# Performance work log

Hardware: AMD Instinct MI355X
Metric: run time of the kernel (lower is better)

The kernel has to match this reference:

```python
import jax, jax.numpy as jnp
import numpy as np

# ---- module constants (from init_kwargs) ----
EMBED_DIM = 384
NUM_HYPEREDGES = 128
TOPK = 64
SPATIAL_SHAPE = (16, 32, 32)  # D, H, W -> N = 16384
SPACING = (2.0, 1.0, 1.0)
SPATIAL_WEIGHT = 0.1
B, N, C = 4, 16 * 32 * 32, EMBED_DIM


def _l2norm(x, axis=-1, eps=1e-12):
    n = jnp.linalg.norm(x, axis=axis, keepdims=True)
    return x / jnp.maximum(n, eps)


def _get_3d_coords():
    D, H, W = SPATIAL_SHAPE
    z = jnp.arange(D, dtype=jnp.float32) * SPACING[0]
    y = jnp.arange(H, dtype=jnp.float32) * SPACING[1]
    x = jnp.arange(W, dtype=jnp.float32) * SPACING[2]
    zz, yy, xx = jnp.meshgrid(z, y, x, indexing='ij')
    return jnp.stack([zz, yy, xx], axis=-1).reshape(-1, 3)  # (N, 3)


def setup_inputs() -> dict:
    key = jax.random.key(0)
    k1, k2 = jax.random.split(key)
    node_features = jax.random.normal(k1, (B, N, C), dtype=jnp.float32)
    class_token = jax.random.normal(k2, (1, 1, C), dtype=jnp.float32)
    temperature = jnp.ones((1,), dtype=jnp.float32) * 0.07
    return {"node_features": node_features, "class_token": class_token, "temperature": temperature}


def reference(node_features, class_token, temperature):
    Ne = NUM_HYPEREDGES
    w = SPATIAL_WEIGHT
    temp = temperature[0]

    nodes_n = _l2norm(node_features)                      # (B, N, C)

    # Step 1: center sampling by semantic similarity to class token
    ct_n = _l2norm(jnp.broadcast_to(class_token, (B, 1, C)))
    scores = jnp.einsum('boc,bnc->bn', ct_n, nodes_n) / temp  # (B, N)
    _, center_idx = jax.lax.top_k(scores, Ne)             # (B, Ne)

    # Gather centers and compute cosine sim of every center vs all nodes
    centers = jnp.take_along_axis(node_features, center_idx[:, :, None], axis=1)  # (B, Ne, C)
    centers_n = _l2norm(centers)
    sem_sim = jnp.einsum('bec,bnc->ben', centers_n, nodes_n) / temp  # (B, Ne, N)

    # Spatial bias (normalized distance from each center voxel)
    coords = _get_3d_coords()                             # (N, 3)
    center_coords = coords[center_idx]                    # (B, Ne, 3)
    diff = coords[None, None, :, :] - center_coords[:, :, None, :]  # (B, Ne, N, 3)
    dist = jnp.linalg.norm(diff, axis=-1)                 # (B, Ne, N)
    dist = dist / (jnp.max(dist, axis=-1, keepdims=True) + 1e-8)
    combined = (1.0 - w) * sem_sim + w * (1.0 - dist)     # (B, Ne, N)

    # Per-hyperedge top-K neighbors -> incidence matrix H (B, N, Ne)
    _, nbr_idx = jax.lax.top_k(combined, TOPK)            # (B, Ne, K)
    b_ix = jnp.arange(B)[:, None, None]
    e_ix = jnp.arange(Ne)[None, :, None]
    Hmat = jnp.zeros((B, N, Ne), dtype=node_features.dtype)
    Hmat = Hmat.at[b_ix, nbr_idx, e_ix].set(1.0)
    return Hmat
```

## Files before the change

### kernel.cpp

```cpp
#include <hip/hip_runtime.h>
#include <math.h>

#define BB 4
#define NN 16384
#define CC 384
#define NE 128
#define KK 64
#define CAP 1024

typedef unsigned short ushort_t;
typedef __attribute__((ext_vector_type(8))) short bf16x8;
typedef __attribute__((ext_vector_type(4))) float f32x4;
#define MFMA(a, b, c) __builtin_amdgcn_mfma_f32_16x16x32_bf16(a, b, c, 0, 0, 0)

__device__ inline unsigned fkey(float f) {
    unsigned b = __float_as_uint(f);
    return (b & 0x80000000u) ? ~b : (b | 0x80000000u);
}
__device__ inline ushort_t bf16rne(float f) {
    unsigned u = __float_as_uint(f);
    unsigned r = u + 0x7FFFu + ((u >> 16) & 1u);
    return (ushort_t)(r >> 16);
}
__device__ inline float bf16tof(ushort_t h) {
    return __uint_as_float(((unsigned)h) << 16);
}
__device__ inline void cvt2(float fa, float fb, unsigned& hp, unsigned& lp) {
    unsigned ua = __float_as_uint(fa), ub = __float_as_uint(fb);
    unsigned ra = ua + 0x8000u, rb = ub + 0x8000u;
    hp = (ra >> 16) | (rb & 0xFFFF0000u);
    float ha = __uint_as_float(ra & 0xFFFF0000u);
    float hb = __uint_as_float(rb & 0xFFFF0000u);
    float la = fa - ha, lb = fb - hb;
    unsigned lra = __float_as_uint(la) + 0x8000u;
    unsigned lrb = __float_as_uint(lb) + 0x8000u;
    lp = (lra >> 16) | (lrb & 0xFFFF0000u);
}

__device__ inline void load_lds16(const ushort_t* g, ushort_t* l) {
    __builtin_amdgcn_global_load_lds(
        (const __attribute__((address_space(1))) unsigned int*)(const void*)g,
        (__attribute__((address_space(3))) unsigned int*)(void*)l, 16, 0, 0);
}

__device__ inline void bin_select4k(const unsigned* hist, int t, int* wsum,
                                    int* sh_bin, int* sh_r, int r) {
    int base = t * 4;
    int c0 = hist[base], c1 = hist[base + 1], c2 = hist[base + 2], c3 = hist[base + 3];
    int csum = c0 + c1 + c2 + c3;
    int lane = t & 63, wid = t >> 6;
    int x = csum;
#pragma unroll
    for (int off = 1; off < 64; off <<= 1) {
        int v = __shfl_down(x, off, 64);
        if (lane + off < 64) x += v;
    }
    if (lane == 0) wsum[wid] = x;
    __syncthreads();
    int after = 0;
    for (int w2 = wid + 1; w2 < 16; ++w2) after += wsum[w2];
    int S = x - csum + after;
    if (S < r && S + c3 >= r) { *sh_bin = base + 3; *sh_r = r - S; }
    S += c3;
    if (S < r && S + c2 >= r) { *sh_bin = base + 2; *sh_r = r - S; }
    S += c2;
    if (S < r && S + c1 >= r) { *sh_bin = base + 1; *sh_r = r - S; }
    S += c1;
    if (S < r && S + c0 >= r) { *sh_bin = base + 0; *sh_r = r - S; }
    __syncthreads();
}

__global__ __launch_bounds__(256) void k_scores(const float* __restrict__ nf,
                                                const float* __restrict__ ct,
                                                unsigned* __restrict__ keys,
                                                float* __restrict__ invn) {
    int wave = threadIdx.x >> 6;
    int lane = threadIdx.x & 63;
    float4 ta = ((const float4*)ct)[lane];
    float2 tc = ((const float2*)(ct + 256))[lane];
    for (int rg = blockIdx.x; rg < BB * NN / 4; rg += gridDim.x) {
        int row = rg * 4 + wave;
        const float* x = nf + (size_t)row * CC;
        float4 a  = ((const float4*)x)[lane];
        float2 c2 = ((const float2*)(x + 256))[lane];
        float ss = a.x*a.x + a.y*a.y + a.z*a.z + a.w*a.w + c2.x*c2.x + c2.y*c2.y;
        float dt = ta.x*a.x + ta.y*a.y + ta.z*a.z + ta.w*a.w + tc.x*c2.x + tc.y*c2.y;
#pragma unroll
        for (int off = 32; off; off >>= 1) {
            ss += __shfl_xor(ss, off, 64);
            dt += __shfl_xor(dt, off, 64);
        }
        if (lane == 0) {
            float inv = 1.0f / fmaxf(sqrtf(ss), 1e-12f);
            invn[row] = inv;
            keys[row] = fkey(dt * inv);
        }
    }
}

__global__ __launch_bounds__(1024) void k_top128(const unsigned* __restrict__ keys,
                                                 const float* __restrict__ nf,
                                                 const float* __restrict__ invn,
                                                 float* __restrict__ meta,
                                                 ushort_t* __restrict__ Ahi,
                                                 ushort_t* __restrict__ Alo) {
    __shared__ unsigned hist[4096];
    __shared__ int wsum[16];
    __shared__ int sh_bin, sh_r;
    __shared__ unsigned cu[NE];
    __shared__ int cil[NE];
    __shared__ unsigned eqk[CAP];
    __shared__ int eqi[CAP];
    __shared__ int cnt_gt, cnt_eq;
    __shared__ int ocid[NE];
    int b = blockIdx.x;
    int t = threadIdx.x;
    const uint4* rowv = (const uint4*)(keys + b * NN);
    if (t == 0) { cnt_gt = 0; cnt_eq = 0; }
    ((uint4*)hist)[t] = make_uint4(0, 0, 0, 0);
    __syncthreads();
    uint4 u0 = rowv[t], u1 = rowv[t + 1024], u2 = rowv[t + 2048], u3 = rowv[t + 3072];
    atomicAdd(&hist[u0.x >> 20], 1u); atomicAdd(&hist[u0.y >> 20], 1u);
    atomicAdd(&hist[u0.z >> 20], 1u); atomicAdd(&hist[u0.w >> 20], 1u);
    atomicAdd(&hist[u1.x >> 20], 1u); atomicAdd(&hist[u1.y >> 20], 1u);
    atomicAdd(&hist[u1.z >> 20], 1u); atomicAdd(&hist[u1.w >> 20], 1u);
    atomicAdd(&hist[u2.x >> 20], 1u); atomicAdd(&hist[u2.y >> 20], 1u);
    atomicAdd(&hist[u2.z >> 20], 1u); atomicAdd(&hist[u2.w >> 20], 1u);
    atomicAdd(&hist[u3.x >> 20], 1u); atomicAdd(&hist[u3.y >> 20], 1u);
    atomicAdd(&hist[u3.z >> 20], 1u); atomicAdd(&hist[u3.w >> 20], 1u);
    __syncthreads();
    bin_select4k(hist, t, wsum, &sh_bin, &sh_r, NE);
    unsigned bin = (unsigned)sh_bin;
    int r = sh_r;
#define EMIT128(uu, nn) { unsigned tb = (uu) >> 20; \
    if (tb > bin) { int p = atomicAdd(&cnt_gt, 1); cu[p] = (uu); cil[p] = (nn); } \
    else if (tb == bin) { int p = atomicAdd(&cnt_eq, 1); if (p < CAP) { eqk[p] = (uu); eqi[p] = (nn); } } }
    EMIT128(u0.x, 4*t+0); EMIT128(u0.y, 4*t+1); EMIT128(u0.z, 4*t+2); EMIT128(u0.w, 4*t+3);
    EMIT128(u1.x, 4096+4*t+0); EMIT128(u1.y, 4096+4*t+1); EMIT128(u1.z, 4096+4*t+2); EMIT128(u1.w, 4096+4*t+3);
    EMIT128(u2.x, 8192+4*t+0); EMIT128(u2.y, 8192+4*t+1); EMIT128(u2.z, 8192+4*t+2); EMIT128(u2.w, 8192+4*t+3);
    EMIT128(u3.x, 12288+4*t+0); EMIT128(u3.y, 12288+4*t+1); EMIT128(u3.z, 12288+4*t+2); EMIT128(u3.w, 12288+4*t+3);
#undef EMIT128
    __syncthreads();
    int ne = cnt_eq < CAP ? cnt_eq : CAP;
    for (int i = t; i < ne; i += 1024) {
        unsigned ki = eqk[i]; int ii = eqi[i], rk = 0;
        for (int j = 0; j < ne; ++j) {
            unsigned kj = eqk[j];
            rk += (kj > ki) || (kj == ki && eqi[j] < ii);
        }
        if (rk < r) { cu[cnt_gt + rk] = ki; cil[cnt_gt + rk] = ii; }
    }
    __syncthreads();
    if (t < NE) {
        unsigned mu = cu[t]; int mi = cil[t], rk = 0;
#pragma unroll 4
        for (int j = 0; j < NE; ++j) {
            unsigned ou = cu[j]; int oi = cil[j];
            rk += (ou > mu) || (ou == mu && oi < mi);
        }
        ocid[rk] = mi;
    }
    __syncthreads();
    if (t < NE) {
        int ci = ocid[t];
        float zc = (float)(ci >> 10) * 2.0f;
        float yc = (float)((ci >> 5) & 31);
        float xc = (float)(ci & 31);
        float mz = fmaxf(zc * zc, (30.f - zc) * (30.f - zc));
        float my = fmaxf(yc * yc, (31.f - yc) * (31.f - yc));
        float mx = fmaxf(xc * xc, (31.f - xc) * (31.f - xc));
        float md = sqrtf(mz + my + mx);
        int be = b * NE + t;
        meta[be * 4 + 0] = zc;
        meta[be * 4 + 1] = yc;
        meta[be * 4 + 2] = xc;
        meta[be * 4 + 3] = 1.0f / (md + 1e-8f);
    }
    {
        int wid2 = t >> 6, lane2 = t & 63;
        ushort_t* dh = Ahi + (size_t)b * NE * CC;
        ushort_t* dl = Alo + (size_t)b * NE * CC;
        for (int e = wid2; e < NE; e += 16) {
            int ci = ocid[e];
            float inv = invn[b * NN + ci];
            const float* src = nf + ((size_t)b * NN + ci) * CC;
            float4 a  = ((const float4*)src)[lane2];
            float2 cv = ((const float2*)(src + 256))[lane2];
            a.x *= inv; a.y *= inv; a.z *= inv; a.w *= inv;
            cv.x *= inv; cv.y *= inv;
            ushort4 h4; ushort2 h2;
            h4.x = bf16rne(a.x); h4.y = bf16rne(a.y); h4.z = bf16rne(a.z); h4.w = bf16rne(a.w);
            h2.x = bf16rne(cv.x); h2.y = bf16rne(cv.y);
            ushort4 l4; ushort2 l2;
            l4.x = bf16rne(a.x - bf16tof(h4.x)); l4.y = bf16rne(a.y - bf16tof(h4.y));
            l4.z = bf16rne(a.z - bf16tof(h4.z)); l4.w = bf16rne(a.w - bf16tof(h4.w));
            l2.x = bf16rne(cv.x - bf16tof(h2.x)); l2.y = bf16rne(cv.y - bf16tof(h2.y));
            int off4 = ((lane2 >> 1) * NE + e) * 8 + 4 * (lane2 & 1);
            int off2 = ((32 + (lane2 >> 2)) * NE + e) * 8 + 2 * (lane2 & 3);
            *(ushort4*)(dh + off4) = h4;
            *(ushort2*)(dh + off2) = h2;
            *(ushort4*)(dl + off4) = l4;
            *(ushort2*)(dl + off2) = l2;
        }
    }
}

__global__ __launch_bounds__(256, 2) void k_gemm(const float* __restrict__ nf,
                                                 const ushort_t* __restrict__ Ahi,
                                                 const ushort_t* __restrict__ Alo,
                                                 const float* __restrict__ invn,
                                                 const float* __restrict__ meta,
                                                 const float* __restrict__ temp,
                                                 unsigned* __restrict__ outk) {
    __shared__ ushort_t Ah[2][4096], Al[2][4096];
    __shared__ ushort_t Bh[2][4160], Bl[2][4160];
    __shared__ float ms[NE * 4];
    __shared__ float invs_s[128];
    int b  = blockIdx.y;
    int n0 = blockIdx.x * 128;
    int t  = threadIdx.x;
    int w = t >> 6, lane = t & 63, quad = lane >> 4, mrow = lane & 15;
    int wr = w >> 1, wc = w & 1;
    for (int i = t; i < NE * 4; i += 256) ms[i] = meta[b * NE * 4 + i];
    if (t < 128) invs_s[t] = invn[b * NN + n0 + t];
    f32x4 acc[4][4];
#pragma unroll
    for (int i = 0; i < 4; ++i)
#pragma unroll
        for (int j = 0; j < 4; ++j) acc[i][j] = (f32x4)0.f;
    const ushort_t* Abh = Ahi + (size_t)b * NE * CC;
    const ushort_t* Abl = Alo + (size_t)b * NE * CC;
    const ushort_t* ah0 = Abh + w * 1024 + lane * 8;
    const ushort_t* ah1 = ah0 + 512;
    const ushort_t* al0 = Abl + w * 1024 + lane * 8;
    const ushort_t* al1 = al0 + 512;
    int bn = t >> 2, bk8 = t & 3;
    int sb0 = bk8 * 130 + bn, sb1 = sb0 + 64;
    const float* bs0 = nf + ((size_t)b * NN + n0 + bn) * CC + bk8 * 8;
    const float* bs1 = bs0 + (size_t)64 * CC;
    float4 s0a, s0b, s0c, s0d;
    float4 s1a, s1b, s1c, s1d;
    load_lds16(ah0, &Ah[0][w * 1024]);
    load_lds16(ah1, &Ah[0][w * 1024 + 512]);
    load_lds16(al0, &Al[0][w * 1024]);
    load_lds16(al1, &Al[0][w * 1024 + 512]);
    __builtin_amdgcn_sched_barrier(0);
    s0a = ((const float4*)bs0)[0]; s0b = ((const float4*)bs0)[1];
    s0c = ((const float4*)bs1)[0]; s0d = ((const float4*)bs1)[1];
    s1a = ((const float4*)(bs0 + 32))[0]; s1b = ((const float4*)(bs0 + 32))[1];
    s1c = ((const float4*)(bs1 + 32))[0]; s1d = ((const float4*)(bs1 + 32))[1];
    {
        uint4 ph, pl;
        cvt2(s0a.x, s0a.y, ph.x, pl.x); cvt2(s0a.z, s0a.w, ph.y, pl.y);
        cvt2(s0b.x, s0b.y, ph.z, pl.z); cvt2(s0b.z, s0b.w, ph.w, pl.w);
        *(uint4*)&Bh[0][sb0 * 8] = ph; *(uint4*)&Bl[0][sb0 * 8] = pl;
        cvt2(s0c.x, s0c.y, ph.x, pl.x); cvt2(s0c.z, s0c.w, ph.y, pl.y);
        cvt2(s0d.x, s0d.y, ph.z, pl.z); cvt2(s0d.z, s0d.w, ph.w, pl.w);
        *(uint4*)&Bh[0][sb1 * 8] = ph; *(uint4*)&Bl[0][sb1 * 8] = pl;
    }
    s0a = ((const float4*)(bs0 + 64))[0]; s0b = ((const float4*)(bs0 + 64))[1];
    s0c = ((const float4*)(bs1 + 64))[0]; s0d = ((const float4*)(bs1 + 64))[1];
    asm volatile("s_waitcnt vmcnt(8) lgkmcnt(0)" ::: "memory");
    __builtin_amdgcn_s_barrier();
    __builtin_amdgcn_sched_barrier(0);

#define GSTEP(KS, CUR, NXT, SA, SB, SC, SD)                                     \
    {                                                                           \
        if ((KS) < 11) {                                                        \
            const int kt = ((KS) + 1) * 32;                                     \
            load_lds16(ah0 + kt * 128, &Ah[NXT][w * 1024]);                     \
            load_lds16(ah1 + kt * 128, &Ah[NXT][w * 1024 + 512]);               \
            load_lds16(al0 + kt * 128, &Al[NXT][w * 1024]);                     \
            load_lds16(al1 + kt * 128, &Al[NXT][w * 1024 + 512]);               \
            __builtin_amdgcn_sched_barrier(0);                                  \
            uint4 ph, pl;                                                       \
            cvt2(SA.x, SA.y, ph.x, pl.x); cvt2(SA.z, SA.w, ph.y, pl.y);         \
            cvt2(SB.x, SB.y, ph.z, pl.z); cvt2(SB.z, SB.w, ph.w, pl.w);         \
            *(uint4*)&Bh[NXT][sb0 * 8] = ph; *(uint4*)&Bl[NXT][sb0 * 8] = pl;   \
            cvt2(SC.x, SC.y, ph.x, pl.x); cvt2(SC.z, SC.w, ph.y, pl.y);         \
            cvt2(SD.x, SD.y, ph.z, pl.z); cvt2(SD.z, SD.w, ph.w, pl.w);         \
            *(uint4*)&Bh[NXT][sb1 * 8] = ph; *(uint4*)&Bl[NXT][sb1 * 8] = pl;   \
            const int kt3 = ((KS) + 3 <= 11 ? (KS) + 3 : 11) * 32;              \
            SA = ((const float4*)(bs0 + kt3))[0];                               \
            SB = ((const float4*)(bs0 + kt3))[1];                               \
            SC = ((const float4*)(bs1 + kt3))[0];                               \
            SD = ((const float4*)(bs1 + kt3))[1];                               \
        }                                                                       \
        bf16x8 afh[4], afl[4], bfh[4], bfl[4];                                  \
        _Pragma("unroll") for (int i = 0; i < 4; ++i) {                         \
            int m = wr * 64 + i * 16 + mrow;                                    \
            afh[i] = *(const bf16x8*)&Ah[CUR][(quad * 128 + m) * 8];            \
            afl[i] = *(const bf16x8*)&Al[CUR][(quad * 128 + m) * 8];            \
        }                                                                       \
        _Pragma("unroll") for (int j = 0; j < 4; ++j) {                         \
            int n = wc * 64 + j * 16 + mrow;                                    \
            bfh[j] = *(const bf16x8*)&Bh[CUR][(quad * 130 + n) * 8];            \
            bfl[j] = *(const bf16x8*)&Bl[CUR][(quad * 130 + n) * 8];            \
        }                                                                       \
        __builtin_amdgcn_s_setprio(1);                                          \
        _Pragma("unroll") for (int i = 0; i < 4; ++i)                           \
        _Pragma("unroll") for (int j = 0; j < 4; ++j) {                         \
            acc[i][j] = MFMA(afh[i], bfh[j], acc[i][j]);                        \
            acc[i][j] = MFMA(afh[i], bfl[j], acc[i][j]);                        \
            acc[i][j] = MFMA(afl[i], bfh[j], acc[i][j]);                        \
        }                                                                       \
        __builtin_amdgcn_s_setprio(0);                                          \
        if ((KS) < 11) {                                                        \
            asm volatile("s_waitcnt vmcnt(8) lgkmcnt(0)" ::: "memory");         \
            __builtin_amdgcn_s_barrier();                                       \
            __builtin_amdgcn_sched_barrier(0);                                  \
        }                                                                       \
    }

    GSTEP(0, 0, 1, s1a, s1b, s1c, s1d)
    GSTEP(1, 1, 0, s0a, s0b, s0c, s0d)
    GSTEP(2, 0, 1, s1a, s1b, s1c, s1d)
    GSTEP(3, 1, 0, s0a, s0b, s0c, s0d)
    GSTEP(4, 0, 1, s1a, s1b, s1c, s1d)
    GSTEP(5, 1, 0, s0a, s0b, s0c, s0d)
    GSTEP(6, 0, 1, s1a, s1b, s1c, s1d)
    GSTEP(7, 1, 0, s0a, s0b, s0c, s0d)
    GSTEP(8, 0, 1, s1a, s1b, s1c, s1d)
    GSTEP(9, 1, 0, s0a, s0b, s0c, s0d)
    GSTEP(10, 0, 1, s1a, s1b, s1c, s1d)
    GSTEP(11, 1, 0, s0a, s0b, s0c, s0d)
#undef GSTEP

    float scale = 0.9f / temp[0];
#pragma unroll
    for (int j = 0; j < 4; ++j) {
        int nloc = wc * 64 + j * 16 + mrow;
        int n = n0 + nloc;
        float invnn = invs_s[nloc];
        float zf = (float)(n >> 10) * 2.0f;
        float yf = (float)((n >> 5) & 31);
        float xf = (float)(n & 31);
#pragma unroll
        for (int i = 0; i < 4; ++i) {
#pragma unroll
            for (int r = 0; r < 4; ++r) {
                int el = wr * 64 + i * 16 + quad * 4 + r;
                float zc = ms[el * 4 + 0], yc = ms[el * 4 + 1], xc = ms[el * 4 + 2], ivd = ms[el * 4 + 3];
                float dz = zf - zc, dy = yf - yc, dx = xf - xc;
                float dist = sqrtf(dz * dz + dy * dy + dx * dx);
                float v = scale * invnn * acc[i][j][r] + 0.1f * (1.0f - dist * ivd);
                outk[((size_t)(b * NE + el)) * NN + n] = fkey(v);
            }
        }
    }
}

__global__ __launch_bounds__(1024) void k_top64(const unsigned* __restrict__ comb,
                                                unsigned* __restrict__ bmg) {
    __shared__ unsigned hist[4096];
    __shared__ unsigned bm[512];
    __shared__ int wsum[16];
    __shared__ int sh_bin, sh_r;
    __shared__ unsigned eqk[CAP];
    __shared__ int eqi[CAP];
    __shared__ int cnt_eq;
    int be = blockIdx.x;
    int t  = threadIdx.x;
    const uint4* rowv = (const uint4*)(comb + (size_t)be * NN);
    if (t == 0) cnt_eq = 0;
    ((uint4*)hist)[t] = make_uint4(0, 0, 0, 0);
    if (t < 128) ((uint4*)bm)[t] = make_uint4(0, 0, 0, 0);
    __syncthreads();
    uint4 u0 = rowv[t], u1 = rowv[t + 1024], u2 = rowv[t + 2048], u3 = rowv[t + 3072];
    atomicAdd(&hist[u0.x >> 20], 1u); atomicAdd(&hist[u0.y >> 20], 1u);
    atomicAdd(&hist[u0.z >> 20], 1u); atomicAdd(&hist[u0.w >> 20], 1u);
    atomicAdd(&hist[u1.x >> 20], 1u); atomicAdd(&hist[u1.y >> 20], 1u);
    atomicAdd(&hist[u1.z >> 20], 1u); atomicAdd(&hist[u1.w >> 20], 1u);
    atomicAdd(&hist[u2.x >> 20], 1u); atomicAdd(&hist[u2.y >> 20], 1u);
    atomicAdd(&hist[u2.z >> 20], 1u); atomicAdd(&hist[u2.w >> 20], 1u);
    atomicAdd(&hist[u3.x >> 20], 1u); atomicAdd(&hist[u3.y >> 20], 1u);
    atomicAdd(&hist[u3.z >> 20], 1u); atomicAdd(&hist[u3.w >> 20], 1u);
    __syncthreads();
    bin_select4k(hist, t, wsum, &sh_bin, &sh_r, KK);
    unsigned bin = (unsigned)sh_bin;
    int r = sh_r;
#define EMIT64(uu, nn) { unsigned tb = (uu) >> 20; \
    if (tb > bin) { atomicOr(&bm[(nn) >> 5], 1u << ((nn) & 31)); } \
    else if (tb == bin) { int p = atomicAdd(&cnt_eq, 1); if (p < CAP) { eqk[p] = (uu); eqi[p] = (nn); } } }
    EMIT64(u0.x, 4*t+0); EMIT64(u0.y, 4*t+1); EMIT64(u0.z, 4*t+2); EMIT64(u0.w, 4*t+3);
    EMIT64(u1.x, 4096+4*t+0); EMIT64(u1.y, 4096+4*t+1); EMIT64(u1.z, 4096+4*t+2); EMIT64(u1.w, 4096+4*t+3);
    EMIT64(u2.x, 8192+4*t+0); EMIT64(u2.y, 8192+4*t+1); EMIT64(u2.z, 8192+4*t+2); EMIT64(u2.w, 8192+4*t+3);
    EMIT64(u3.x, 12288+4*t+0); EMIT64(u3.y, 12288+4*t+1); EMIT64(u3.z, 12288+4*t+2); EMIT64(u3.w, 12288+4*t+3);
#undef EMIT64
    __syncthreads();
    int ne = cnt_eq < CAP ? cnt_eq : CAP;
    for (int i = t; i < ne; i += 1024) {
        unsigned ki = eqk[i]; int ii = eqi[i], rk = 0;
        for (int j = 0; j < ne; ++j) {
            unsigned kj = eqk[j];
            rk += (kj > ki) || (kj == ki && eqi[j] < ii);
        }
        if (rk < r) atomicOr(&bm[ii >> 5], 1u << (ii & 31));
    }
    __syncthreads();
    if (t < 128) ((uint4*)(bmg + (size_t)be * 512))[t] = ((uint4*)bm)[t];
}

__global__ __launch_bounds__(256) void k_expand(const unsigned* __restrict__ bmg,
                                                float* __restrict__ H) {
    __shared__ unsigned wl[256];
    int b  = blockIdx.y;
    int n0 = blockIdx.x * 64;
    int t  = threadIdx.x;
    int w0 = n0 >> 5;
    wl[t] = bmg[((size_t)b * NE + (t >> 1)) * 512 + w0 + (t & 1)];
    __syncthreads();
    float4* dst = (float4*)(H + ((size_t)b * NN + n0) * NE);
#pragma unroll
    for (int i = 0; i < 8; ++i) {
        int flat = t + 256 * i;
        int nl = flat >> 5, f4 = flat & 31;
        int wsel = nl >> 5, bit = nl & 31;
        int e = f4 * 4;
        float4 v;
        v.x = (float)((wl[(e + 0) * 2 + wsel] >> bit) & 1u);
        v.y = (float)((wl[(e + 1) * 2 + wsel] >> bit) & 1u);
        v.z = (float)((wl[(e + 2) * 2 + wsel] >> bit) & 1u);
        v.w = (float)((wl[(e + 3) * 2 + wsel] >> bit) & 1u);
        dst[flat] = v;
    }
}

extern "C" void kernel_launch(void* const* d_in, const int* in_sizes, int n_in,
                              void* d_out, int out_size, void* d_ws, size_t ws_size,
                              hipStream_t stream) {
    const float* nf   = (const float*)d_in[0];
    const float* ct   = (const float*)d_in[1];
    const float* temp = (const float*)d_in[2];
    float* out = (float*)d_out;

    unsigned* keys = (unsigned*)d_ws;
    float* invn    = (float*)(keys + BB * NN);
    float* meta    = invn + BB * NN;
    ushort_t* Ahi  = (ushort_t*)(meta + BB * NE * 4);
    ushort_t* Alo  = Ahi + (size_t)BB * NE * CC;
    unsigned* bmg  = (unsigned*)(Alo + (size_t)BB * NE * CC);

    k_scores <<<2048, 256, 0, stream>>>(nf, ct, keys, invn);
    k_top128 <<<BB, 1024, 0, stream>>>(keys, nf, invn, meta, Ahi, Alo);
    k_gemm   <<<dim3(NN / 128, BB), 256, 0, stream>>>(nf, Ahi, Alo, invn, meta, temp, (unsigned*)out);
    k_top64  <<<BB * NE, 1024, 0, stream>>>((const unsigned*)out, bmg);
    k_expand <<<dim3(NN / 64, BB), 256, 0, stream>>>(bmg, out);
}
```

Baseline: 245.3 us.

## Pre-split node features into bf16 hi/lo tiles in k_scores, stream into GEMM via LDS loads

k_scores, which already reads every node row, now also splits each fp32 feature into bf16 hi/lo parts and writes them to workspace in the exact tiled layout the GEMM consumes. k_gemm then loads both A and B operands with direct global-to-LDS loads and no longer does in-loop conversion or register staging. The aim is to take conversion ALU work and scattered fp32 loads off the GEMM's critical path. The cost is extra global writes of the hi/lo copies (same byte count as the fp32 input), which k_gemm reads back. The wait now drains all outstanding loads (vmcnt(0)) at each step.

Result: slower. 309.6 us (+26.2%).

```diff
diff --git a/kernel.cpp b/kernel.cpp
--- a/kernel.cpp
+++ b/kernel.cpp
@@ -73,11 +73,15 @@
 __global__ __launch_bounds__(256) void k_scores(const float* __restrict__ nf,
                                                 const float* __restrict__ ct,
                                                 unsigned* __restrict__ keys,
-                                                float* __restrict__ invn) {
+                                                float* __restrict__ invn,
+                                                ushort_t* __restrict__ Bhi,
+                                                ushort_t* __restrict__ Blo) {
     int wave = threadIdx.x >> 6;
     int lane = threadIdx.x & 63;
     float4 ta = ((const float4*)ct)[lane];
     float2 tc = ((const float2*)(ct + 256))[lane];
+    int off4 = ((lane >> 1) * 128) * 8 + 4 * (lane & 1);
+    int off2 = ((32 + (lane >> 2)) * 128) * 8 + 2 * (lane & 3);
     for (int rg = blockIdx.x; rg < BB * NN / 4; rg += gridDim.x) {
         int row = rg * 4 + wave;
         const float* x = nf + (size_t)row * CC;
@@ -95,6 +99,18 @@
             invn[row] = inv;
             keys[row] = fkey(dt * inv);
         }
+        uint2 h4, l4; unsigned h2, l2;
+        cvt2(a.x, a.y, h4.x, l4.x);
+        cvt2(a.z, a.w, h4.y, l4.y);
+        cvt2(c2.x, c2.y, h2, l2);
+        int bq = row >> 14;
+        int n  = row & (NN - 1);
+        int nt = n >> 7, nl = n & 127;
+        size_t tb = ((size_t)(bq * 128 + nt)) * 49152;
+        *(uint2*)(Bhi + tb + off4 + nl * 8) = h4;
+        *(uint2*)(Blo + tb + off4 + nl * 8) = l4;
+        *(unsigned*)(Bhi + tb + off2 + nl * 8) = h2;
+        *(unsigned*)(Blo + tb + off2 + nl * 8) = l2;
     }
 }
 
@@ -205,19 +221,21 @@
     }
 }
 
-__global__ __launch_bounds__(256, 2) void k_gemm(const float* __restrict__ nf,
-                                                 const ushort_t* __restrict__ Ahi,
+__global__ __launch_bounds__(256, 2) void k_gemm(const ushort_t* __restrict__ Ahi,
                                                  const ushort_t* __restrict__ Alo,
+                                                 const ushort_t* __restrict__ Bhi,
+                                                 const ushort_t* __restrict__ Blo,
                                                  const float* __restrict__ invn,
                                                  const float* __restrict__ meta,
                                                  const float* __restrict__ temp,
                                                  unsigned* __restrict__ outk) {
     __shared__ ushort_t Ah[2][4096], Al[2][4096];
-    __shared__ ushort_t Bh[2][4160], Bl[2][4160];
+    __shared__ ushort_t Bh[2][4096], Bl[2][4096];
     __shared__ float ms[NE * 4];
     __shared__ float invs_s[128];
     int b  = blockIdx.y;
-    int n0 = blockIdx.x * 128;
+    int bx = blockIdx.x;
+    int n0 = bx * 128;
     int t  = threadIdx.x;
     int w = t >> 6, lane = t & 63, quad = lane >> 4, mrow = lane & 15;
     int wr = w >> 1, wc = w & 1;
@@ -228,104 +246,67 @@
     for (int i = 0; i < 4; ++i)
 #pragma unroll
         for (int j = 0; j < 4; ++j) acc[i][j] = (f32x4)0.f;
-    const ushort_t* Abh = Ahi + (size_t)b * NE * CC;
-    const ushort_t* Abl = Alo + (size_t)b * NE * CC;
-    const ushort_t* ah0 = Abh + w * 1024 + lane * 8;
-    const ushort_t* ah1 = ah0 + 512;
-    const ushort_t* al0 = Abl + w * 1024 + lane * 8;
-    const ushort_t* al1 = al0 + 512;
-    int bn = t >> 2, bk8 = t & 3;
-    int sb0 = bk8 * 130 + bn, sb1 = sb0 + 64;
-    const float* bs0 = nf + ((size_t)b * NN + n0 + bn) * CC + bk8 * 8;
-    const float* bs1 = bs0 + (size_t)64 * CC;
-    float4 s0a, s0b, s0c, s0d;
-    float4 s1a, s1b, s1c, s1d;
-    load_lds16(ah0, &Ah[0][w * 1024]);
-    load_lds16(ah1, &Ah[0][w * 1024 + 512]);
-    load_lds16(al0, &Al[0][w * 1024]);
-    load_lds16(al1, &Al[0][w * 1024 + 512]);
-    __builtin_amdgcn_sched_barrier(0);
-    s0a = ((const float4*)bs0)[0]; s0b = ((const float4*)bs0)[1];
-    s0c = ((const float4*)bs1)[0]; s0d = ((const float4*)bs1)[1];
-    s1a = ((const float4*)(bs0 + 32))[0]; s1b = ((const float4*)(bs0 + 32))[1];
-    s1c = ((const float4*)(bs1 + 32))[0]; s1d = ((const float4*)(bs1 + 32))[1];
-    {
-        uint4 ph, pl;
-        cvt2(s0a.x, s0a.y, ph.x, pl.x); cvt2(s0a.z, s0a.w, ph.y, pl.y);
-        cvt2(s0b.x, s0b.y, ph.z, pl.z); cvt2(s0b.z, s0b.w, ph.w, pl.w);
-        *(uint4*)&Bh[0][sb0 * 8] = ph; *(uint4*)&Bl[0][sb0 * 8] = pl;
-        cvt2(s0c.x, s0c.y, ph.x, pl.x); cvt2(s0c.z, s0c.w, ph.y, pl.y);
-        cvt2(s0d.x, s0d.y, ph.z, pl.z); cvt2(s0d.z, s0d.w, ph.w, pl.w);
-        *(uint4*)&Bh[0][sb1 * 8] = ph; *(uint4*)&Bl[0][sb1 * 8] = pl;
-    }
-    s0a = ((const float4*)(bs0 + 64))[0]; s0b = ((const float4*)(bs0 + 64))[1];
-    s0c = ((const float4*)(bs1 + 64))[0]; s0d = ((const float4*)(bs1 + 64))[1];
-    asm volatile("s_waitcnt vmcnt(8) lgkmcnt(0)" ::: "memory");
+    const ushort_t* Asrh = Ahi + (size_t)b * NE * CC + w * 1024 + lane * 8;
+    const ushort_t* Asrl = Alo + (size_t)b * NE * CC + w * 1024 + lane * 8;
+    const ushort_t* Bsrh = Bhi + ((size_t)(b * 128 + bx)) * 49152 + w * 1024 + lane * 8;
+    const ushort_t* Bsrl = Blo + ((size_t)(b * 128 + bx)) * 49152 + w * 1024 + lane * 8;
+    int ld0 = w * 1024, ld1 = w * 1024 + 512;
+    load_lds16(Asrh,       &Ah[0][ld0]);
+    load_lds16(Asrh + 512, &Ah[0][ld1]);
+    load_lds16(Asrl,       &Al[0][ld0]);
+    load_lds16(Asrl + 512, &Al[0][ld1]);
+    load_lds16(Bsrh,       &Bh[0][ld0]);
+    load_lds16(Bsrh + 512, &Bh[0][ld1]);
+    load_lds16(Bsrl,       &Bl[0][ld0]);
+    load_lds16(Bsrl + 512, &Bl[0][ld1]);
+    asm volatile("s_waitcnt vmcnt(0)" ::: "memory");
     __builtin_amdgcn_s_barrier();
     __builtin_amdgcn_sched_barrier(0);
-
-#define GSTEP(KS, CUR, NXT, SA, SB, SC, SD)                                     \
-    {                                                                           \
-        if ((KS) < 11) {                                                        \
-            const int kt = ((KS) + 1) * 32;                                     \
-            load_lds16(ah0 + kt * 128, &Ah[NXT][w * 1024]);                     \
-            load_lds16(ah1 + kt * 128, &Ah[NXT][w * 1024 + 512]);               \
-            load_lds16(al0 + kt * 128, &Al[NXT][w * 1024]);                     \
-            load_lds16(al1 + kt * 128, &Al[NXT][w * 1024 + 512]);               \
-            __builtin_amdgcn_sched_barrier(0);                                  \
-            uint4 ph, pl;                                                       \
-            cvt2(SA.x, SA.y, ph.x, pl.x); cvt2(SA.z, SA.w, ph.y, pl.y);         \
-            cvt2(SB.x, SB.y, ph.z, pl.z); cvt2(SB.z, SB.w, ph.w, pl.w);         \
-            *(uint4*)&Bh[NXT][sb0 * 8] = ph; *(uint4*)&Bl[NXT][sb0 * 8] = pl;   \
-            cvt2(SC.x, SC.y, ph.x, pl.x); cvt2(SC.z, SC.w, ph.y, pl.y);         \
-            cvt2(SD.x, SD.y, ph.z, pl.z); cvt2(SD.z, SD.w, ph.w, pl.w);         \
-            *(uint4*)&Bh[NXT][sb1 * 8] = ph; *(uint4*)&Bl[NXT][sb1 * 8] = pl;   \
-            const int kt3 = ((KS) + 3 <= 11 ? (KS) + 3 : 11) * 32;              \
-            SA = ((const float4*)(bs0 + kt3))[0];                               \
-            SB = ((const float4*)(bs0 + kt3))[1];                               \
-            SC = ((const float4*)(bs1 + kt3))[0];                               \
-            SD = ((const float4*)(bs1 + kt3))[1];                               \
-        }                                                                       \
-        bf16x8 afh[4], afl[4], bfh[4], bfl[4];                                  \
-        _Pragma("unroll") for (int i = 0; i < 4; ++i) {                         \
-            int m = wr * 64 + i * 16 + mrow;                                    \
-            afh[i] = *(const bf16x8*)&Ah[CUR][(quad * 128 + m) * 8];            \
-            afl[i] = *(const bf16x8*)&Al[CUR][(quad * 128 + m) * 8];            \
-        }                                                                       \
-        _Pragma("unroll") for (int j = 0; j < 4; ++j) {                         \
-            int n = wc * 64 + j * 16 + mrow;                                    \
-            bfh[j] = *(const bf16x8*)&Bh[CUR][(quad * 130 + n) * 8];            \
-            bfl[j] = *(const bf16x8*)&Bl[CUR][(quad * 130 + n) * 8];            \
-        }                                                                       \
-        __builtin_amdgcn_s_setprio(1);                                          \
-        _Pragma("unroll") for (int i = 0; i < 4; ++i)                           \
-        _Pragma("unroll") for (int j = 0; j < 4; ++j) {                         \
-            acc[i][j] = MFMA(afh[i], bfh[j], acc[i][j]);                        \
-            acc[i][j] = MFMA(afh[i], bfl[j], acc[i][j]);                        \
-            acc[i][j] = MFMA(afl[i], bfh[j], acc[i][j]);                        \
-        }                                                                       \
-        __builtin_amdgcn_s_setprio(0);                                          \
-        if ((KS) < 11) {                                                        \
-            asm volatile("s_waitcnt vmcnt(8) lgkmcnt(0)" ::: "memory");         \
-            __builtin_amdgcn_s_barrier();                                       \
-            __builtin_amdgcn_sched_barrier(0);                                  \
-        }                                                                       \
-    }
-
-    GSTEP(0, 0, 1, s1a, s1b, s1c, s1d)
-    GSTEP(1, 1, 0, s0a, s0b, s0c, s0d)
-    GSTEP(2, 0, 1, s1a, s1b, s1c, s1d)
-    GSTEP(3, 1, 0, s0a, s0b, s0c, s0d)
-    GSTEP(4, 0, 1, s1a, s1b, s1c, s1d)
-    GSTEP(5, 1, 0, s0a, s0b, s0c, s0d)
-    GSTEP(6, 0, 1, s1a, s1b, s1c, s1d)
-    GSTEP(7, 1, 0, s0a, s0b, s0c, s0d)
-    GSTEP(8, 0, 1, s1a, s1b, s1c, s1d)
-    GSTEP(9, 1, 0, s0a, s0b, s0c, s0d)
-    GSTEP(10, 0, 1, s1a, s1b, s1c, s1d)
-    GSTEP(11, 1, 0, s0a, s0b, s0c, s0d)
-#undef GSTEP
-
+    int cur = 0;
+    for (int ks = 0; ks < 12; ++ks) {
+        int nxt = cur ^ 1;
+        if (ks < 11) {
+            int so = (ks + 1) * 4096;
+            load_lds16(Asrh + so,       &Ah[nxt][ld0]);
+            load_lds16(Asrh + so + 512, &Ah[nxt][ld1]);
+            load_lds16(Asrl + so,       &Al[nxt][ld0]);
+            load_lds16(Asrl + so + 512, &Al[nxt][ld1]);
+            load_lds16(Bsrh + so,       &Bh[nxt][ld0]);
+            load_lds16(Bsrh + so + 512, &Bh[nxt][ld1]);
+            load_lds16(Bsrl + so,       &Bl[nxt][ld0]);
+            load_lds16(Bsrl + so + 512, &Bl[nxt][ld1]);
+            __builtin_amdgcn_sched_barrier(0);
+        }
+        bf16x8 afh[4], afl[4], bfh[4], bfl[4];
+#pragma unroll
+        for (int i = 0; i < 4; ++i) {
+            int m = wr * 64 + i * 16 + mrow;
+            afh[i] = *(const bf16x8*)&Ah[cur][(quad * 128 + m) * 8];
+            afl[i] = *(const bf16x8*)&Al[cur][(quad * 128 + m) * 8];
+        }
+#pragma unroll
+        for (int j = 0; j < 4; ++j) {
+            int n = wc * 64 + j * 16 + mrow;
+            bfh[j] = *(const bf16x8*)&Bh[cur][(quad * 128 + n) * 8];
+            bfl[j] = *(const bf16x8*)&Bl[cur][(quad * 128 + n) * 8];
+        }
+        __builtin_amdgcn_s_setprio(1);
+#pragma unroll
+        for (int i = 0; i < 4; ++i)
+#pragma unroll
+            for (int j = 0; j < 4; ++j) {
+                acc[i][j] = MFMA(afh[i], bfh[j], acc[i][j]);
+                acc[i][j] = MFMA(afh[i], bfl[j], acc[i][j]);
+                acc[i][j] = MFMA(afl[i], bfh[j], acc[i][j]);
+            }
+        __builtin_amdgcn_s_setprio(0);
+        if (ks < 11) {
+            asm volatile("s_waitcnt vmcnt(0) lgkmcnt(0)" ::: "memory");
+            __builtin_amdgcn_s_barrier();
+            __builtin_amdgcn_sched_barrier(0);
+        }
+        cur = nxt;
+    }
     float scale = 0.9f / temp[0];
 #pragma unroll
     for (int j = 0; j < 4; ++j) {
@@ -440,10 +421,12 @@
     ushort_t* Ahi  = (ushort_t*)(meta + BB * NE * 4);
     ushort_t* Alo  = Ahi + (size_t)BB * NE * CC;
     unsigned* bmg  = (unsigned*)(Alo + (size_t)BB * NE * CC);
-
-    k_scores <<<2048, 256, 0, stream>>>(nf, ct, keys, invn);
+    ushort_t* Bhi  = (ushort_t*)(bmg + (size_t)BB * NE * 512);
+    ushort_t* Blo  = Bhi + (size_t)BB * NN * CC;
+
+    k_scores <<<2048, 256, 0, stream>>>(nf, ct, keys, invn, Bhi, Blo);
     k_top128 <<<BB, 1024, 0, stream>>>(keys, nf, invn, meta, Ahi, Alo);
-    k_gemm   <<<dim3(NN / 128, BB), 256, 0, stream>>>(nf, Ahi, Alo, invn, meta, temp, (unsigned*)out);
+    k_gemm   <<<dim3(NN / 128, BB), 256, 0, stream>>>(Ahi, Alo, Bhi, Blo, invn, meta, temp, (unsigned*)out);
     k_top64  <<<BB * NE, 1024, 0, stream>>>((const unsigned*)out, bmg);
     k_expand <<<dim3(NN / 64, BB), 256, 0, stream>>>(bmg, out);
 }
```
